# Kernel tuning notes

Measured on AMD Instinct MI355X. Metric: run time of the kernel, lower is better.

Reference implementation:

```python
import jax, jax.numpy as jnp
import numpy as np

LEN_HIS = 20   # q_len_his: sliding-window history length
DIM_C = 4      # dim_c
H = 64         # GRU hidden = final_mlp_hidden_width
D = 36         # global_graph_width(32) + goal(2) + action(2)
N = 32768      # total timesteps across many episodes


def setup_inputs() -> dict:
    key = jax.random.key(0)
    ks = jax.random.split(key, 8)
    emb = jax.random.normal(ks[0], (N, D), jnp.float32)
    dones = (jax.random.uniform(ks[1], (N, 1)) < 0.02).astype(jnp.int32)
    s = lambda k, shape, fan: jax.random.normal(k, shape, jnp.float32) / np.sqrt(fan).astype(np.float32)
    return {
        "embeddings": emb,
        "W_ih": s(ks[2], (3 * H, D), D),
        "W_hh": s(ks[3], (3 * H, H), H),
        "b_ih": jnp.zeros((3 * H,), jnp.float32),
        "b_hh": jnp.zeros((3 * H,), jnp.float32),
        "W1": s(ks[4], (H, H), H),
        "b1": jnp.zeros((H,), jnp.float32),
        "W2": s(ks[5], (DIM_C, H), H),
        "b2": jnp.zeros((DIM_C,), jnp.float32),
        "dones": dones,
    }


def _his_calculate_c(embeddings, W_ih, W_hh, b_ih, b_hh, W1, b1, W2, b2, dones):
    """Batched/padded version of the ragged sliding-window GRU+MLP loop.

    For each timestep t, the torch code runs the GRU over
    embeddings[max(episode_start, t-L+1) : t+1] from a zero hidden state,
    then applies FinalPredMLP to the final hidden state.
    """
    n = embeddings.shape[0]
    done = dones[:, 0] != 0
    idx = jnp.arange(n)
    # episode_start[t] = (index of most recent done strictly before t) + 1, else 0
    prev_done = jnp.concatenate([jnp.zeros((1,), bool), done[:-1]])
    ep_start = jax.lax.cummax(jnp.where(prev_done, idx, 0))
    win_start = jnp.maximum(ep_start, idx - LEN_HIS + 1)            # [N]

    # padded windows: position l holds embeddings[t - (L-1) + l]
    gidx = idx[:, None] - (LEN_HIS - 1) + jnp.arange(LEN_HIS)[None, :]  # [N, L]
    valid = gidx >= win_start[:, None]                                   # [N, L]
    X = embeddings[jnp.clip(gidx, 0, n - 1)] * valid[..., None]          # [N, L, D]

    def cell(h, inp):
        x, v = inp                      # x: [N, D], v: [N]
        gi = x @ W_ih.T + b_ih          # [N, 3H]
        gh = h @ W_hh.T + b_hh          # [N, 3H]
        ir, iz, inn = jnp.split(gi, 3, axis=-1)
        hr, hz, hnn = jnp.split(gh, 3, axis=-1)
        r = jax.nn.sigmoid(ir + hr)
        z = jax.nn.sigmoid(iz + hz)
        ncand = jnp.tanh(inn + r * hnn)
        h_new = (1.0 - z) * ncand + z * h
        return jnp.where(v[:, None], h_new, h), None

    h0 = jnp.zeros((n, H), embeddings.dtype)
    hT, _ = jax.lax.scan(cell, h0, (jnp.swapaxes(X, 0, 1), valid.T))  # [N, H]

    # FinalPredMLP: Linear(H,H) -> ReLU -> Linear(H, dim_c)
    hid = jax.nn.relu(hT @ W1.T + b1)
    return hid @ W2.T + b2              # [N, dim_c]


def reference(embeddings, W_ih, W_hh, b_ih, b_hh, W1, b1, W2, b2, dones):
    return _his_calculate_c(embeddings, W_ih, W_hh, b_ih, b_hh, W1, b1, W2, b2, dones)
```

## Files before the change

### kernel.cpp

```cpp
#include <hip/hip_runtime.h>

#define NT 32768
#define DI 36
#define HH 64
#define LH 20
#define TPB 32
#define NROW 51
#define SGS 196
#define EMBS 40

#define NLOG2E -1.4426950408889634f
#define TLOG2E 2.8853900817779268f

#define UNION_OFF  39984
#define SFIRST_OFF 49200
#define SMEM_BYTES 49328

typedef __attribute__((ext_vector_type(8))) short bf16x8;
typedef __attribute__((ext_vector_type(4))) float f32x4;
typedef __attribute__((ext_vector_type(4))) int int4v;
union frag_cast { int4v i4; bf16x8 h8; };

__device__ __forceinline__ unsigned f2u(float f) { union { float f; unsigned u; } x; x.f = f; return x.u; }
__device__ __forceinline__ float u2f(unsigned u) { union { float f; unsigned u; } x; x.u = u; return x.f; }
__device__ __forceinline__ unsigned short f2bf_rne(float f) {
    union { float f; unsigned u; } x; x.f = f;
    unsigned r = x.u + 0x7FFFu + ((x.u >> 16) & 1u);
    return (unsigned short)(r >> 16);
}

__global__ __launch_bounds__(64) void prep_kernel(
    const float* __restrict__ W_ih, const float* __restrict__ W_hh,
    const float* __restrict__ W1, int4v* __restrict__ wfrag)
{
    const int b = (int)blockIdx.x;
    const int l = (int)threadIdx.x;
    unsigned short e[8];
    if (b < 72) {
        const int set = b / 24, fb = b % 24;
        const int mt = fb >> 1, kt = fb & 1;
        const int m = mt * 16 + (l & 15);
        const float sc = ((mt >> 2) < 2) ? NLOG2E : TLOG2E;
        const int k0 = kt * 32 + (l >> 4) * 8;
#pragma unroll
        for (int jj = 0; jj < 8; ++jj) {
            const int k = k0 + jj;
            if (set == 2) {
                e[jj] = f2bf_rne(W_hh[(size_t)m * HH + k] * sc);
            } else {
                const float v = (k < DI) ? W_ih[(size_t)m * DI + k] * sc : 0.f;
                const unsigned u = f2u(v);
                if (set == 0) e[jj] = (unsigned short)(u >> 16);
                else          e[jj] = (unsigned short)(f2u(v - u2f(u & 0xFFFF0000u)) >> 16);
            }
        }
    } else {
        const int bb = b - 72;
        const bool is_lo = bb >= 8;
        const int f = bb & 7;
        const int mt = f >> 1, kt = f & 1;
        const int m = mt * 16 + (l & 15);
        const int k0 = kt * 32 + (l >> 4) * 8;
#pragma unroll
        for (int jj = 0; jj < 8; ++jj) {
            const float v = W1[(size_t)m * HH + k0 + jj];
            const unsigned u = f2u(v);
            if (!is_lo) e[jj] = (unsigned short)(u >> 16);
            else        e[jj] = (unsigned short)(f2u(v - u2f(u & 0xFFFF0000u)) >> 16);
        }
    }
    int4v p;
    p.x = e[0] | ((unsigned)e[1] << 16); p.y = e[2] | ((unsigned)e[3] << 16);
    p.z = e[4] | ((unsigned)e[5] << 16); p.w = e[6] | ((unsigned)e[7] << 16);
    wfrag[b * 64 + l] = p;
}

__global__ __launch_bounds__(256, 3) void gru_kernel(
    const float* __restrict__ emb, const int4v* __restrict__ wfrag,
    const float* __restrict__ b_ih, const float* __restrict__ b_hh,
    const float* __restrict__ b1, const float* __restrict__ W2,
    const float* __restrict__ b2, const int* __restrict__ dones,
    float* __restrict__ out)
{
    __shared__ __align__(16) char SMEM[SMEM_BYTES];
    float* const Sg = (float*)SMEM;
    unsigned short* const EmbH = (unsigned short*)(SMEM + UNION_OFF);
    unsigned short* const EmbL = EmbH + NROW * EMBS;
    unsigned short* const HbB  = (unsigned short*)(SMEM + UNION_OFF);
    unsigned short* const HfH  = (unsigned short*)(SMEM + UNION_OFF);
    unsigned short* const HfL  = HfH + 2304;
    int* const sfirst = (int*)(SMEM + SFIRST_OFF);

    const int tid = threadIdx.x;
    const int lane = tid & 63;
    const int W = tid >> 6;
    const int li = lane & 15;
    const int q = lane >> 4;
    const int blk = ((int)blockIdx.x & 7) * 128 + ((int)blockIdx.x >> 3);
    const int T0 = blk * TPB;

    {
        int4v* z = (int4v*)EmbH;
        for (int i = tid; i < 510; i += 256) z[i] = int4v{0, 0, 0, 0};
    }
    if (tid < TPB) {
        const int tt = T0 + tid;
        int lo = tt - (LH - 1); if (lo < 0) lo = 0;
        int ws = lo;
        for (int j = lo; j < tt; ++j)
            ws = (dones[j] != 0) ? (j + 1) : ws;
        sfirst[tid] = ws - (tt - (LH - 1));
    }
    __syncthreads();
    for (int i = tid; i < NROW * DI; i += 256) {
        const int r = i / DI, c = i % DI;
        int tt = T0 - (LH - 1) + r; tt = tt < 0 ? 0 : tt;
        const float v = emb[(size_t)tt * DI + c];
        const unsigned u = f2u(v);
        EmbH[r * EMBS + c] = (unsigned short)(u >> 16);
        EmbL[r * EMBS + c] = (unsigned short)(f2u(v - u2f(u & 0xFFFF0000u)) >> 16);
    }

    bf16x8 aih[3][2], ail[3][2], whh[3][2];
#pragma unroll
    for (int g = 0; g < 3; ++g)
#pragma unroll
        for (int kt = 0; kt < 2; ++kt) {
            const int fb = (4 * g + W) * 2 + kt;
            frag_cast a, b, c;
            a.i4 = wfrag[(0 * 24 + fb) * 64 + lane];
            b.i4 = wfrag[(1 * 24 + fb) * 64 + lane];
            c.i4 = wfrag[(2 * 24 + fb) * 64 + lane];
            aih[g][kt] = a.h8; ail[g][kt] = b.h8; whh[g][kt] = c.h8;
        }

    const int joff = 16 * W + 4 * q;
    f32x4 biasI[3];
#pragma unroll
    for (int g = 0; g < 3; ++g) {
        const float sc = (g < 2) ? NLOG2E : TLOG2E;
        const f32x4 bi = *(const f32x4*)&b_ih[64 * g + joff];
        if (g < 2) {
            const f32x4 bh = *(const f32x4*)&b_hh[64 * g + joff];
#pragma unroll
            for (int rr = 0; rr < 4; ++rr) biasI[g][rr] = (bi[rr] + bh[rr]) * sc;
        } else {
#pragma unroll
            for (int rr = 0; rr < 4; ++rr) biasI[g][rr] = bi[rr] * sc;
        }
    }
    f32x4 bnv;
    {
        const f32x4 b = *(const f32x4*)&b_hh[128 + joff];
#pragma unroll
        for (int rr = 0; rr < 4; ++rr) bnv[rr] = b[rr] * TLOG2E;
    }
    __syncthreads();

#pragma unroll
    for (int nt = 0; nt < 4; ++nt) {
        const int row = ((nt == 3) ? 35 : 16 * nt) + li;
        bf16x8 ebh0 = *(const bf16x8*)&EmbH[row * EMBS + 8 * q];
        bf16x8 ebl0 = *(const bf16x8*)&EmbL[row * EMBS + 8 * q];
        bf16x8 ebh1 = bf16x8{0, 0, 0, 0, 0, 0, 0, 0};
        bf16x8 ebl1 = bf16x8{0, 0, 0, 0, 0, 0, 0, 0};
        if (q == 0) {
            ebh1 = *(const bf16x8*)&EmbH[row * EMBS + 32];
            ebl1 = *(const bf16x8*)&EmbL[row * EMBS + 32];
        }
#pragma unroll
        for (int g = 0; g < 3; ++g) {
            f32x4 a = biasI[g];
            a = __builtin_amdgcn_mfma_f32_16x16x32_bf16(aih[g][0], ebh0, a, 0, 0, 0);
            a = __builtin_amdgcn_mfma_f32_16x16x32_bf16(aih[g][1], ebh1, a, 0, 0, 0);
            a = __builtin_amdgcn_mfma_f32_16x16x32_bf16(ail[g][0], ebh0, a, 0, 0, 0);
            a = __builtin_amdgcn_mfma_f32_16x16x32_bf16(ail[g][1], ebh1, a, 0, 0, 0);
            a = __builtin_amdgcn_mfma_f32_16x16x32_bf16(aih[g][0], ebl0, a, 0, 0, 0);
            a = __builtin_amdgcn_mfma_f32_16x16x32_bf16(aih[g][1], ebl1, a, 0, 0, 0);
            *(f32x4*)&Sg[row * SGS + 64 * g + joff] = a;
        }
    }
    __syncthreads();
    const int sfr[2] = { sfirst[li], sfirst[16 + li] };

    float h[2][4];
    f32x4 gv0[2], gv1[2], gv2[2];

    {
#pragma unroll
        for (int nt = 0; nt < 2; ++nt) {
            const float* gp = Sg + (16 * nt + li) * SGS;
            const f32x4 aR = *(const f32x4*)(gp + joff);
            const f32x4 aZ = *(const f32x4*)(gp + 64 + joff);
            const f32x4 gI = *(const f32x4*)(gp + 128 + joff);
            const bool valid = (0 >= sfr[nt]);
#pragma unroll
            for (int rr = 0; rr < 4; ++rr) {
                const float r  = __builtin_amdgcn_rcpf(1.f + __builtin_amdgcn_exp2f(aR[rr]));
                const float z  = __builtin_amdgcn_rcpf(1.f + __builtin_amdgcn_exp2f(aZ[rr]));
                const float nc = 1.f - 2.f * __builtin_amdgcn_rcpf(1.f + __builtin_amdgcn_exp2f(gI[rr] + r * bnv[rr]));
                h[nt][rr] = valid ? fmaf(z, 0.f - nc, nc) : 0.f;
            }
            uint2 ph;
            ph.x = __builtin_amdgcn_perm(f2u(h[nt][1]), f2u(h[nt][0]), 0x07060302u);
            ph.y = __builtin_amdgcn_perm(f2u(h[nt][3]), f2u(h[nt][2]), 0x07060302u);
            *(uint2*)&HbB[2304 + (16 * nt + li) * 72 + joff] = ph;
            const float* gq = Sg + (16 * nt + li + 1) * SGS;
            gv0[nt] = *(const f32x4*)(gq + joff);
            gv1[nt] = *(const f32x4*)(gq + 64 + joff);
            gv2[nt] = *(const f32x4*)(gq + 128 + joff);
        }
    }
    __syncthreads();

#pragma unroll 2
    for (int s = 1; s < LH; ++s) {
        const int rb = s & 1;
        bf16x8 bh0[2], bh1[2];
#pragma unroll
        for (int nt = 0; nt < 2; ++nt) {
            bh0[nt] = *(const bf16x8*)&HbB[rb * 2304 + (16 * nt + li) * 72 + 8 * q];
            bh1[nt] = *(const bf16x8*)&HbB[rb * 2304 + (16 * nt + li) * 72 + 32 + 8 * q];
        }
        f32x4 aR[2], aZ[2], aN[2], gI[2];
#pragma unroll
        for (int nt = 0; nt < 2; ++nt) {
            aR[nt] = gv0[nt]; aZ[nt] = gv1[nt]; gI[nt] = gv2[nt]; aN[nt] = bnv;
        }
#pragma unroll
        for (int nt = 0; nt < 2; ++nt) {
            int r = 16 * nt + li + s + 1; r = r > NROW - 1 ? NROW - 1 : r;
            const float* gq = Sg + r * SGS;
            gv0[nt] = *(const f32x4*)(gq + joff);
            gv1[nt] = *(const f32x4*)(gq + 64 + joff);
            gv2[nt] = *(const f32x4*)(gq + 128 + joff);
        }
#pragma unroll
        for (int nt = 0; nt < 2; ++nt) {
            aR[nt] = __builtin_amdgcn_mfma_f32_16x16x32_bf16(whh[0][0], bh0[nt], aR[nt], 0, 0, 0);
            aR[nt] = __builtin_amdgcn_mfma_f32_16x16x32_bf16(whh[0][1], bh1[nt], aR[nt], 0, 0, 0);
            aZ[nt] = __builtin_amdgcn_mfma_f32_16x16x32_bf16(whh[1][0], bh0[nt], aZ[nt], 0, 0, 0);
            aZ[nt] = __builtin_amdgcn_mfma_f32_16x16x32_bf16(whh[1][1], bh1[nt], aZ[nt], 0, 0, 0);
            aN[nt] = __builtin_amdgcn_mfma_f32_16x16x32_bf16(whh[2][0], bh0[nt], aN[nt], 0, 0, 0);
            aN[nt] = __builtin_amdgcn_mfma_f32_16x16x32_bf16(whh[2][1], bh1[nt], aN[nt], 0, 0, 0);
        }
#pragma unroll
        for (int nt = 0; nt < 2; ++nt) {
            const bool valid = (s >= sfr[nt]);
#pragma unroll
            for (int rr = 0; rr < 4; ++rr) {
                const float r  = __builtin_amdgcn_rcpf(1.f + __builtin_amdgcn_exp2f(aR[nt][rr]));
                const float z  = __builtin_amdgcn_rcpf(1.f + __builtin_amdgcn_exp2f(aZ[nt][rr]));
                const float nc = 1.f - 2.f * __builtin_amdgcn_rcpf(1.f + __builtin_amdgcn_exp2f(gI[nt][rr] + r * aN[nt][rr]));
                const float hn = fmaf(z, h[nt][rr] - nc, nc);
                h[nt][rr] = valid ? hn : h[nt][rr];
            }
            if (s != LH - 1) {
                uint2 ph;
                ph.x = __builtin_amdgcn_perm(f2u(h[nt][1]), f2u(h[nt][0]), 0x07060302u);
                ph.y = __builtin_amdgcn_perm(f2u(h[nt][3]), f2u(h[nt][2]), 0x07060302u);
                *(uint2*)&HbB[(1 - rb) * 2304 + (16 * nt + li) * 72 + joff] = ph;
            }
        }
        __syncthreads();
    }

#pragma unroll
    for (int nt = 0; nt < 2; ++nt) {
        const unsigned u0 = f2u(h[nt][0]), u1 = f2u(h[nt][1]);
        const unsigned u2 = f2u(h[nt][2]), u3 = f2u(h[nt][3]);
        uint2 ph, pl;
        ph.x = __builtin_amdgcn_perm(u1, u0, 0x07060302u);
        ph.y = __builtin_amdgcn_perm(u3, u2, 0x07060302u);
        const unsigned l0 = f2u(h[nt][0] - u2f(u0 & 0xFFFF0000u));
        const unsigned l1 = f2u(h[nt][1] - u2f(u1 & 0xFFFF0000u));
        const unsigned l2 = f2u(h[nt][2] - u2f(u2 & 0xFFFF0000u));
        const unsigned l3 = f2u(h[nt][3] - u2f(u3 & 0xFFFF0000u));
        pl.x = __builtin_amdgcn_perm(l1, l0, 0x07060302u);
        pl.y = __builtin_amdgcn_perm(l3, l2, 0x07060302u);
        *(uint2*)&HfH[(16 * nt + li) * 72 + joff] = ph;
        *(uint2*)&HfL[(16 * nt + li) * 72 + joff] = pl;
    }
    __syncthreads();
    {
        bf16x8 w1h[2], w1l[2];
#pragma unroll
        for (int kt = 0; kt < 2; ++kt) {
            frag_cast a, b;
            a.i4 = wfrag[(72 + W * 2 + kt) * 64 + lane];
            b.i4 = wfrag[(80 + W * 2 + kt) * 64 + lane];
            w1h[kt] = a.h8; w1l[kt] = b.h8;
        }
        const f32x4 bb1 = *(const f32x4*)&b1[joff];
#pragma unroll
        for (int nt = 0; nt < 2; ++nt) {
            const int t = 16 * nt + li;
            const bf16x8 bh0 = *(const bf16x8*)&HfH[t * 72 + 8 * q];
            const bf16x8 bh1 = *(const bf16x8*)&HfH[t * 72 + 32 + 8 * q];
            const bf16x8 bl0 = *(const bf16x8*)&HfL[t * 72 + 8 * q];
            const bf16x8 bl1 = *(const bf16x8*)&HfL[t * 72 + 32 + 8 * q];
            f32x4 a = bb1;
            a = __builtin_amdgcn_mfma_f32_16x16x32_bf16(w1h[0], bh0, a, 0, 0, 0);
            a = __builtin_amdgcn_mfma_f32_16x16x32_bf16(w1h[1], bh1, a, 0, 0, 0);
            a = __builtin_amdgcn_mfma_f32_16x16x32_bf16(w1l[0], bh0, a, 0, 0, 0);
            a = __builtin_amdgcn_mfma_f32_16x16x32_bf16(w1l[1], bh1, a, 0, 0, 0);
            a = __builtin_amdgcn_mfma_f32_16x16x32_bf16(w1h[0], bl0, a, 0, 0, 0);
            a = __builtin_amdgcn_mfma_f32_16x16x32_bf16(w1h[1], bl1, a, 0, 0, 0);
            float4 st;
            st.x = fmaxf(a[0], 0.f); st.y = fmaxf(a[1], 0.f);
            st.z = fmaxf(a[2], 0.f); st.w = fmaxf(a[3], 0.f);
            *(float4*)&Sg[t * 68 + joff] = st;
        }
    }
    __syncthreads();
    if (tid < 128) {
        const int tt = tid >> 2, c = tid & 3;
        float o2 = b2[c];
#pragma unroll
        for (int m4 = 0; m4 < 16; ++m4) {
            const float4 hv = *(const float4*)&Sg[tt * 68 + 4 * m4];
            const float4 wv = *(const float4*)&W2[c * HH + 4 * m4];
            o2 += hv.x * wv.x + hv.y * wv.y + hv.z * wv.z + hv.w * wv.w;
        }
        out[(size_t)(T0 + tt) * 4 + c] = o2;
    }
}

extern "C" void kernel_launch(void* const* d_in, const int* in_sizes, int n_in,
                              void* d_out, int out_size, void* d_ws, size_t ws_size,
                              hipStream_t stream) {
    const float* emb  = (const float*)d_in[0];
    const float* W_ih = (const float*)d_in[1];
    const float* W_hh = (const float*)d_in[2];
    const float* b_ih = (const float*)d_in[3];
    const float* b_hh = (const float*)d_in[4];
    const float* W1   = (const float*)d_in[5];
    const float* b1   = (const float*)d_in[6];
    const float* W2   = (const float*)d_in[7];
    const float* b2   = (const float*)d_in[8];
    const int*   dn   = (const int*)d_in[9];

    int4v* wfrag = (int4v*)d_ws;
    float* o = (float*)d_out;

    prep_kernel<<<88, 64, 0, stream>>>(W_ih, W_hh, W1, wfrag);
    gru_kernel<<<NT / TPB, 256, 0, stream>>>(emb, wfrag, b_ih, b_hh,
                                             b1, W2, b2, dn, o);
}
```

Measured before the change: 113.1 us.

## Give each wave its own timesteps so the GRU recurrence runs without block barriers

Result: no change. 112.4 us (-0.6%).

```diff
diff --git a/kernel.cpp b/kernel.cpp
--- a/kernel.cpp
+++ b/kernel.cpp
@@ -4,17 +4,17 @@
 #define DI 36
 #define HH 64
 #define LH 20
-#define TPB 32
-#define NROW 51
+#define TPB 64
+#define NROW 83
 #define SGS 196
 #define EMBS 40
 
 #define NLOG2E -1.4426950408889634f
 #define TLOG2E 2.8853900817779268f
 
-#define UNION_OFF  39984
-#define SFIRST_OFF 49200
-#define SMEM_BYTES 49328
+#define UNION_OFF  65072
+#define SFIRST_OFF 78352
+#define SMEM_BYTES 78608
 
 typedef __attribute__((ext_vector_type(8))) short bf16x8;
 typedef __attribute__((ext_vector_type(4))) float f32x4;
@@ -75,7 +75,7 @@
     wfrag[b * 64 + l] = p;
 }
 
-__global__ __launch_bounds__(256, 3) void gru_kernel(
+__global__ __launch_bounds__(256, 2) void gru_kernel(
     const float* __restrict__ emb, const int4v* __restrict__ wfrag,
     const float* __restrict__ b_ih, const float* __restrict__ b_hh,
     const float* __restrict__ b1, const float* __restrict__ W2,
@@ -86,9 +86,7 @@
     float* const Sg = (float*)SMEM;
     unsigned short* const EmbH = (unsigned short*)(SMEM + UNION_OFF);
     unsigned short* const EmbL = EmbH + NROW * EMBS;
-    unsigned short* const HbB  = (unsigned short*)(SMEM + UNION_OFF);
-    unsigned short* const HfH  = (unsigned short*)(SMEM + UNION_OFF);
-    unsigned short* const HfL  = HfH + 2304;
+    unsigned short* const Hb   = (unsigned short*)(SMEM + UNION_OFF);
     int* const sfirst = (int*)(SMEM + SFIRST_OFF);
 
     const int tid = threadIdx.x;
@@ -96,12 +94,12 @@
     const int W = tid >> 6;
     const int li = lane & 15;
     const int q = lane >> 4;
-    const int blk = ((int)blockIdx.x & 7) * 128 + ((int)blockIdx.x >> 3);
+    const int blk = ((int)blockIdx.x & 7) * 64 + ((int)blockIdx.x >> 3);
     const int T0 = blk * TPB;
 
     {
         int4v* z = (int4v*)EmbH;
-        for (int i = tid; i < 510; i += 256) z[i] = int4v{0, 0, 0, 0};
+        for (int i = tid; i < 830; i += 256) z[i] = int4v{0, 0, 0, 0};
     }
     if (tid < TPB) {
         const int tt = T0 + tid;
@@ -121,17 +119,16 @@
         EmbL[r * EMBS + c] = (unsigned short)(f2u(v - u2f(u & 0xFFFF0000u)) >> 16);
     }
 
-    bf16x8 aih[3][2], ail[3][2], whh[3][2];
+    bf16x8 aih[3][2], ail[3][2];
 #pragma unroll
     for (int g = 0; g < 3; ++g)
 #pragma unroll
         for (int kt = 0; kt < 2; ++kt) {
             const int fb = (4 * g + W) * 2 + kt;
-            frag_cast a, b, c;
+            frag_cast a, b;
             a.i4 = wfrag[(0 * 24 + fb) * 64 + lane];
             b.i4 = wfrag[(1 * 24 + fb) * 64 + lane];
-            c.i4 = wfrag[(2 * 24 + fb) * 64 + lane];
-            aih[g][kt] = a.h8; ail[g][kt] = b.h8; whh[g][kt] = c.h8;
+            aih[g][kt] = a.h8; ail[g][kt] = b.h8;
         }
 
     const int joff = 16 * W + 4 * q;
@@ -149,17 +146,12 @@
             for (int rr = 0; rr < 4; ++rr) biasI[g][rr] = bi[rr] * sc;
         }
     }
-    f32x4 bnv;
-    {
-        const f32x4 b = *(const f32x4*)&b_hh[128 + joff];
-#pragma unroll
-        for (int rr = 0; rr < 4; ++rr) bnv[rr] = b[rr] * TLOG2E;
-    }
     __syncthreads();
 
 #pragma unroll
-    for (int nt = 0; nt < 4; ++nt) {
-        const int row = ((nt == 3) ? 35 : 16 * nt) + li;
+    for (int rt = 0; rt < 6; ++rt) {
+        const int row0 = (rt == 5) ? 67 : 16 * rt;
+        const int row = row0 + li;
         bf16x8 ebh0 = *(const bf16x8*)&EmbH[row * EMBS + 8 * q];
         bf16x8 ebl0 = *(const bf16x8*)&EmbL[row * EMBS + 8 * q];
         bf16x8 ebh1 = bf16x8{0, 0, 0, 0, 0, 0, 0, 0};
@@ -181,149 +173,155 @@
         }
     }
     __syncthreads();
-    const int sfr[2] = { sfirst[li], sfirst[16 + li] };
-
-    float h[2][4];
-    f32x4 gv0[2], gv1[2], gv2[2];
-
+
+    bf16x8 whh[3][4][2];
+#pragma unroll
+    for (int g = 0; g < 3; ++g)
+#pragma unroll
+        for (int mt = 0; mt < 4; ++mt)
+#pragma unroll
+            for (int kt = 0; kt < 2; ++kt) {
+                frag_cast c;
+                c.i4 = wfrag[(48 + (4 * g + mt) * 2 + kt) * 64 + lane];
+                whh[g][mt][kt] = c.h8;
+            }
+    f32x4 bnv4[4];
+#pragma unroll
+    for (int mt = 0; mt < 4; ++mt) {
+        const f32x4 b = *(const f32x4*)&b_hh[128 + 16 * mt + 4 * q];
+#pragma unroll
+        for (int rr = 0; rr < 4; ++rr) bnv4[mt][rr] = b[rr] * TLOG2E;
+    }
+    const int sfr = sfirst[16 * W + li];
+    unsigned short* const Hbw = Hb + W * 1152;
+
+    float h[4][4];
     {
-#pragma unroll
-        for (int nt = 0; nt < 2; ++nt) {
-            const float* gp = Sg + (16 * nt + li) * SGS;
-            const f32x4 aR = *(const f32x4*)(gp + joff);
-            const f32x4 aZ = *(const f32x4*)(gp + 64 + joff);
-            const f32x4 gI = *(const f32x4*)(gp + 128 + joff);
-            const bool valid = (0 >= sfr[nt]);
+        const float* gp = Sg + (16 * W + li) * SGS;
+        const bool valid = (0 >= sfr);
+#pragma unroll
+        for (int mt = 0; mt < 4; ++mt) {
+            const f32x4 aR = *(const f32x4*)(gp + 16 * mt + 4 * q);
+            const f32x4 aZ = *(const f32x4*)(gp + 64 + 16 * mt + 4 * q);
+            const f32x4 gI = *(const f32x4*)(gp + 128 + 16 * mt + 4 * q);
 #pragma unroll
             for (int rr = 0; rr < 4; ++rr) {
                 const float r  = __builtin_amdgcn_rcpf(1.f + __builtin_amdgcn_exp2f(aR[rr]));
                 const float z  = __builtin_amdgcn_rcpf(1.f + __builtin_amdgcn_exp2f(aZ[rr]));
-                const float nc = 1.f - 2.f * __builtin_amdgcn_rcpf(1.f + __builtin_amdgcn_exp2f(gI[rr] + r * bnv[rr]));
-                h[nt][rr] = valid ? fmaf(z, 0.f - nc, nc) : 0.f;
+                const float nc = 1.f - 2.f * __builtin_amdgcn_rcpf(1.f + __builtin_amdgcn_exp2f(gI[rr] + r * bnv4[mt][rr]));
+                h[mt][rr] = valid ? fmaf(z, 0.f - nc, nc) : 0.f;
             }
             uint2 ph;
-            ph.x = __builtin_amdgcn_perm(f2u(h[nt][1]), f2u(h[nt][0]), 0x07060302u);
-            ph.y = __builtin_amdgcn_perm(f2u(h[nt][3]), f2u(h[nt][2]), 0x07060302u);
-            *(uint2*)&HbB[2304 + (16 * nt + li) * 72 + joff] = ph;
-            const float* gq = Sg + (16 * nt + li + 1) * SGS;
-            gv0[nt] = *(const f32x4*)(gq + joff);
-            gv1[nt] = *(const f32x4*)(gq + 64 + joff);
-            gv2[nt] = *(const f32x4*)(gq + 128 + joff);
-        }
-    }
-    __syncthreads();
-
-#pragma unroll 2
+            ph.x = __builtin_amdgcn_perm(f2u(h[mt][1]), f2u(h[mt][0]), 0x07060302u);
+            ph.y = __builtin_amdgcn_perm(f2u(h[mt][3]), f2u(h[mt][2]), 0x07060302u);
+            *(uint2*)&Hbw[li * 72 + 16 * mt + 4 * q] = ph;
+        }
+    }
+
+#pragma unroll 1
     for (int s = 1; s < LH; ++s) {
-        const int rb = s & 1;
-        bf16x8 bh0[2], bh1[2];
-#pragma unroll
-        for (int nt = 0; nt < 2; ++nt) {
-            bh0[nt] = *(const bf16x8*)&HbB[rb * 2304 + (16 * nt + li) * 72 + 8 * q];
-            bh1[nt] = *(const bf16x8*)&HbB[rb * 2304 + (16 * nt + li) * 72 + 32 + 8 * q];
-        }
-        f32x4 aR[2], aZ[2], aN[2], gI[2];
-#pragma unroll
-        for (int nt = 0; nt < 2; ++nt) {
-            aR[nt] = gv0[nt]; aZ[nt] = gv1[nt]; gI[nt] = gv2[nt]; aN[nt] = bnv;
-        }
-#pragma unroll
-        for (int nt = 0; nt < 2; ++nt) {
-            int r = 16 * nt + li + s + 1; r = r > NROW - 1 ? NROW - 1 : r;
-            const float* gq = Sg + r * SGS;
-            gv0[nt] = *(const f32x4*)(gq + joff);
-            gv1[nt] = *(const f32x4*)(gq + 64 + joff);
-            gv2[nt] = *(const f32x4*)(gq + 128 + joff);
-        }
-#pragma unroll
-        for (int nt = 0; nt < 2; ++nt) {
-            aR[nt] = __builtin_amdgcn_mfma_f32_16x16x32_bf16(whh[0][0], bh0[nt], aR[nt], 0, 0, 0);
-            aR[nt] = __builtin_amdgcn_mfma_f32_16x16x32_bf16(whh[0][1], bh1[nt], aR[nt], 0, 0, 0);
-            aZ[nt] = __builtin_amdgcn_mfma_f32_16x16x32_bf16(whh[1][0], bh0[nt], aZ[nt], 0, 0, 0);
-            aZ[nt] = __builtin_amdgcn_mfma_f32_16x16x32_bf16(whh[1][1], bh1[nt], aZ[nt], 0, 0, 0);
-            aN[nt] = __builtin_amdgcn_mfma_f32_16x16x32_bf16(whh[2][0], bh0[nt], aN[nt], 0, 0, 0);
-            aN[nt] = __builtin_amdgcn_mfma_f32_16x16x32_bf16(whh[2][1], bh1[nt], aN[nt], 0, 0, 0);
-        }
-#pragma unroll
-        for (int nt = 0; nt < 2; ++nt) {
-            const bool valid = (s >= sfr[nt]);
+        const bf16x8 bh0 = *(const bf16x8*)&Hbw[li * 72 + 8 * q];
+        const bf16x8 bh1 = *(const bf16x8*)&Hbw[li * 72 + 32 + 8 * q];
+        const float* gp = Sg + (16 * W + li + s) * SGS;
+        f32x4 aR[4], aZ[4], aN[4], gI[4];
+#pragma unroll
+        for (int mt = 0; mt < 4; ++mt) {
+            aR[mt] = *(const f32x4*)(gp + 16 * mt + 4 * q);
+            aZ[mt] = *(const f32x4*)(gp + 64 + 16 * mt + 4 * q);
+            gI[mt] = *(const f32x4*)(gp + 128 + 16 * mt + 4 * q);
+            aN[mt] = bnv4[mt];
+        }
+#pragma unroll
+        for (int mt = 0; mt < 4; ++mt) {
+            aR[mt] = __builtin_amdgcn_mfma_f32_16x16x32_bf16(whh[0][mt][0], bh0, aR[mt], 0, 0, 0);
+            aR[mt] = __builtin_amdgcn_mfma_f32_16x16x32_bf16(whh[0][mt][1], bh1, aR[mt], 0, 0, 0);
+            aZ[mt] = __builtin_amdgcn_mfma_f32_16x16x32_bf16(whh[1][mt][0], bh0, aZ[mt], 0, 0, 0);
+            aZ[mt] = __builtin_amdgcn_mfma_f32_16x16x32_bf16(whh[1][mt][1], bh1, aZ[mt], 0, 0, 0);
+            aN[mt] = __builtin_amdgcn_mfma_f32_16x16x32_bf16(whh[2][mt][0], bh0, aN[mt], 0, 0, 0);
+            aN[mt] = __builtin_amdgcn_mfma_f32_16x16x32_bf16(whh[2][mt][1], bh1, aN[mt], 0, 0, 0);
+        }
+        const bool valid = (s >= sfr);
+#pragma unroll
+        for (int mt = 0; mt < 4; ++mt) {
 #pragma unroll
             for (int rr = 0; rr < 4; ++rr) {
-                const float r  = __builtin_amdgcn_rcpf(1.f + __builtin_amdgcn_exp2f(aR[nt][rr]));
-                const float z  = __builtin_amdgcn_rcpf(1.f + __builtin_amdgcn_exp2f(aZ[nt][rr]));
-                const float nc = 1.f - 2.f * __builtin_amdgcn_rcpf(1.f + __builtin_amdgcn_exp2f(gI[nt][rr] + r * aN[nt][rr]));
-                const float hn = fmaf(z, h[nt][rr] - nc, nc);
-                h[nt][rr] = valid ? hn : h[nt][rr];
+                const float r  = __builtin_amdgcn_rcpf(1.f + __builtin_amdgcn_exp2f(aR[mt][rr]));
+                const float z  = __builtin_amdgcn_rcpf(1.f + __builtin_amdgcn_exp2f(aZ[mt][rr]));
+                const float nc = 1.f - 2.f * __builtin_amdgcn_rcpf(1.f + __builtin_amdgcn_exp2f(gI[mt][rr] + r * aN[mt][rr]));
+                const float hn = fmaf(z, h[mt][rr] - nc, nc);
+                h[mt][rr] = valid ? hn : h[mt][rr];
             }
             if (s != LH - 1) {
                 uint2 ph;
-                ph.x = __builtin_amdgcn_perm(f2u(h[nt][1]), f2u(h[nt][0]), 0x07060302u);
-                ph.y = __builtin_amdgcn_perm(f2u(h[nt][3]), f2u(h[nt][2]), 0x07060302u);
-                *(uint2*)&HbB[(1 - rb) * 2304 + (16 * nt + li) * 72 + joff] = ph;
-            }
-        }
-        __syncthreads();
-    }
-
-#pragma unroll
-    for (int nt = 0; nt < 2; ++nt) {
-        const unsigned u0 = f2u(h[nt][0]), u1 = f2u(h[nt][1]);
-        const unsigned u2 = f2u(h[nt][2]), u3 = f2u(h[nt][3]);
-        uint2 ph, pl;
-        ph.x = __builtin_amdgcn_perm(u1, u0, 0x07060302u);
-        ph.y = __builtin_amdgcn_perm(u3, u2, 0x07060302u);
-        const unsigned l0 = f2u(h[nt][0] - u2f(u0 & 0xFFFF0000u));
-        const unsigned l1 = f2u(h[nt][1] - u2f(u1 & 0xFFFF0000u));
-        const unsigned l2 = f2u(h[nt][2] - u2f(u2 & 0xFFFF0000u));
-        const unsigned l3 = f2u(h[nt][3] - u2f(u3 & 0xFFFF0000u));
+                ph.x = __builtin_amdgcn_perm(f2u(h[mt][1]), f2u(h[mt][0]), 0x07060302u);
+                ph.y = __builtin_amdgcn_perm(f2u(h[mt][3]), f2u(h[mt][2]), 0x07060302u);
+                *(uint2*)&Hbw[li * 72 + 16 * mt + 4 * q] = ph;
+            }
+        }
+    }
+
+    bf16x8 w1h[4][2], w1l[4][2];
+#pragma unroll
+    for (int mt = 0; mt < 4; ++mt)
+#pragma unroll
+        for (int kt = 0; kt < 2; ++kt) {
+            frag_cast a, b;
+            a.i4 = wfrag[(72 + mt * 2 + kt) * 64 + lane];
+            b.i4 = wfrag[(80 + mt * 2 + kt) * 64 + lane];
+            w1h[mt][kt] = a.h8; w1l[mt][kt] = b.h8;
+        }
+#pragma unroll
+    for (int mt = 0; mt < 4; ++mt) {
+        uint2 ph;
+        ph.x = __builtin_amdgcn_perm(f2u(h[mt][1]), f2u(h[mt][0]), 0x07060302u);
+        ph.y = __builtin_amdgcn_perm(f2u(h[mt][3]), f2u(h[mt][2]), 0x07060302u);
+        *(uint2*)&Hbw[li * 72 + 16 * mt + 4 * q] = ph;
+    }
+    const bf16x8 bh0 = *(const bf16x8*)&Hbw[li * 72 + 8 * q];
+    const bf16x8 bh1 = *(const bf16x8*)&Hbw[li * 72 + 32 + 8 * q];
+#pragma unroll
+    for (int mt = 0; mt < 4; ++mt) {
+        const unsigned u0 = f2u(h[mt][0]), u1 = f2u(h[mt][1]);
+        const unsigned u2 = f2u(h[mt][2]), u3 = f2u(h[mt][3]);
+        const unsigned l0 = f2u(h[mt][0] - u2f(u0 & 0xFFFF0000u));
+        const unsigned l1 = f2u(h[mt][1] - u2f(u1 & 0xFFFF0000u));
+        const unsigned l2 = f2u(h[mt][2] - u2f(u2 & 0xFFFF0000u));
+        const unsigned l3 = f2u(h[mt][3] - u2f(u3 & 0xFFFF0000u));
+        uint2 pl;
         pl.x = __builtin_amdgcn_perm(l1, l0, 0x07060302u);
         pl.y = __builtin_amdgcn_perm(l3, l2, 0x07060302u);
-        *(uint2*)&HfH[(16 * nt + li) * 72 + joff] = ph;
-        *(uint2*)&HfL[(16 * nt + li) * 72 + joff] = pl;
-    }
-    __syncthreads();
-    {
-        bf16x8 w1h[2], w1l[2];
-#pragma unroll
-        for (int kt = 0; kt < 2; ++kt) {
-            frag_cast a, b;
-            a.i4 = wfrag[(72 + W * 2 + kt) * 64 + lane];
-            b.i4 = wfrag[(80 + W * 2 + kt) * 64 + lane];
-            w1h[kt] = a.h8; w1l[kt] = b.h8;
-        }
-        const f32x4 bb1 = *(const f32x4*)&b1[joff];
-#pragma unroll
-        for (int nt = 0; nt < 2; ++nt) {
-            const int t = 16 * nt + li;
-            const bf16x8 bh0 = *(const bf16x8*)&HfH[t * 72 + 8 * q];
-            const bf16x8 bh1 = *(const bf16x8*)&HfH[t * 72 + 32 + 8 * q];
-            const bf16x8 bl0 = *(const bf16x8*)&HfL[t * 72 + 8 * q];
-            const bf16x8 bl1 = *(const bf16x8*)&HfL[t * 72 + 32 + 8 * q];
-            f32x4 a = bb1;
-            a = __builtin_amdgcn_mfma_f32_16x16x32_bf16(w1h[0], bh0, a, 0, 0, 0);
-            a = __builtin_amdgcn_mfma_f32_16x16x32_bf16(w1h[1], bh1, a, 0, 0, 0);
-            a = __builtin_amdgcn_mfma_f32_16x16x32_bf16(w1l[0], bh0, a, 0, 0, 0);
-            a = __builtin_amdgcn_mfma_f32_16x16x32_bf16(w1l[1], bh1, a, 0, 0, 0);
-            a = __builtin_amdgcn_mfma_f32_16x16x32_bf16(w1h[0], bl0, a, 0, 0, 0);
-            a = __builtin_amdgcn_mfma_f32_16x16x32_bf16(w1h[1], bl1, a, 0, 0, 0);
-            float4 st;
-            st.x = fmaxf(a[0], 0.f); st.y = fmaxf(a[1], 0.f);
-            st.z = fmaxf(a[2], 0.f); st.w = fmaxf(a[3], 0.f);
-            *(float4*)&Sg[t * 68 + joff] = st;
-        }
-    }
-    __syncthreads();
-    if (tid < 128) {
-        const int tt = tid >> 2, c = tid & 3;
-        float o2 = b2[c];
-#pragma unroll
-        for (int m4 = 0; m4 < 16; ++m4) {
-            const float4 hv = *(const float4*)&Sg[tt * 68 + 4 * m4];
-            const float4 wv = *(const float4*)&W2[c * HH + 4 * m4];
-            o2 += hv.x * wv.x + hv.y * wv.y + hv.z * wv.z + hv.w * wv.w;
-        }
-        out[(size_t)(T0 + tt) * 4 + c] = o2;
-    }
+        *(uint2*)&Hbw[li * 72 + 16 * mt + 4 * q] = pl;
+    }
+    const bf16x8 bl0 = *(const bf16x8*)&Hbw[li * 72 + 8 * q];
+    const bf16x8 bl1 = *(const bf16x8*)&Hbw[li * 72 + 32 + 8 * q];
+
+    float p0 = 0.f, p1 = 0.f, p2 = 0.f, p3 = 0.f;
+#pragma unroll
+    for (int mt = 0; mt < 4; ++mt) {
+        f32x4 a = *(const f32x4*)&b1[16 * mt + 4 * q];
+        a = __builtin_amdgcn_mfma_f32_16x16x32_bf16(w1h[mt][0], bh0, a, 0, 0, 0);
+        a = __builtin_amdgcn_mfma_f32_16x16x32_bf16(w1h[mt][1], bh1, a, 0, 0, 0);
+        a = __builtin_amdgcn_mfma_f32_16x16x32_bf16(w1l[mt][0], bh0, a, 0, 0, 0);
+        a = __builtin_amdgcn_mfma_f32_16x16x32_bf16(w1l[mt][1], bh1, a, 0, 0, 0);
+        a = __builtin_amdgcn_mfma_f32_16x16x32_bf16(w1h[mt][0], bl0, a, 0, 0, 0);
+        a = __builtin_amdgcn_mfma_f32_16x16x32_bf16(w1h[mt][1], bl1, a, 0, 0, 0);
+        const float h0 = fmaxf(a[0], 0.f), h1 = fmaxf(a[1], 0.f);
+        const float h2 = fmaxf(a[2], 0.f), h3 = fmaxf(a[3], 0.f);
+        const f32x4 w0 = *(const f32x4*)&W2[0 * HH + 16 * mt + 4 * q];
+        const f32x4 w1 = *(const f32x4*)&W2[1 * HH + 16 * mt + 4 * q];
+        const f32x4 w2 = *(const f32x4*)&W2[2 * HH + 16 * mt + 4 * q];
+        const f32x4 w3 = *(const f32x4*)&W2[3 * HH + 16 * mt + 4 * q];
+        p0 += h0 * w0[0] + h1 * w0[1] + h2 * w0[2] + h3 * w0[3];
+        p1 += h0 * w1[0] + h1 * w1[1] + h2 * w1[2] + h3 * w1[3];
+        p2 += h0 * w2[0] + h1 * w2[1] + h2 * w2[2] + h3 * w2[3];
+        p3 += h0 * w3[0] + h1 * w3[1] + h2 * w3[2] + h3 * w3[3];
+    }
+    p0 += __shfl_xor(p0, 16); p0 += __shfl_xor(p0, 32);
+    p1 += __shfl_xor(p1, 16); p1 += __shfl_xor(p1, 32);
+    p2 += __shfl_xor(p2, 16); p2 += __shfl_xor(p2, 32);
+    p3 += __shfl_xor(p3, 16); p3 += __shfl_xor(p3, 32);
+    const float pv = (q == 0) ? p0 : (q == 1) ? p1 : (q == 2) ? p2 : p3;
+    out[(size_t)(T0 + 16 * W + li) * 4 + q] = pv + b2[q];
 }
 
 extern "C" void kernel_launch(void* const* d_in, const int* in_sizes, int n_in,
```
